# Kernel optimization log

Hardware: AMD Instinct MI355X
Metric: run time of the kernel (lower is better)

The kernel has to match this reference:

```python
import jax, jax.numpy as jnp
import numpy as np

IGNORE_INDEX = 255
THRESH = 0.7
MIN_KEPT = 100000


def _ohem_ce(predict, target):
    # predict: (n, c, h, w) float logits; target: (n, h, w) int labels
    n, c, h, w = predict.shape
    logits = predict.transpose(0, 2, 3, 1).reshape(-1, c)   # (P, c), P = n*h*w
    labels = target.reshape(-1)                              # (P,)

    valid = labels != IGNORE_INDEX
    safe_labels = jnp.where(valid, labels, 0)

    # stable log-softmax once; prob-at-label = exp(logp-at-label)
    logp = jax.nn.log_softmax(logits, axis=-1)               # (P, c)
    logp_lab = jnp.take_along_axis(logp, safe_labels[:, None], axis=-1)[:, 0]  # (P,)
    pred = jnp.exp(logp_lab)                                 # softmax prob of true class

    num_valid = jnp.sum(valid)

    # k-th smallest prob among valid pixels (selection is not differentiated,
    # matching the torch code which does this on numpy/CPU)
    pred_ng = jax.lax.stop_gradient(pred)
    pred_sel = jnp.where(valid, pred_ng, jnp.inf)
    neg_topk, _ = jax.lax.top_k(-pred_sel, MIN_KEPT)         # MIN_KEPT smallest preds
    kth = -neg_topk[-1]                                      # MIN_KEPT-th smallest

    threshold = jnp.where(kth > THRESH, kth, THRESH)

    # OHEM keep rule only applies when num_valid > min_kept; otherwise keep all valid
    do_ohem = num_valid > MIN_KEPT
    kept = jnp.where(do_ohem, valid & (pred_ng <= threshold), valid)

    cnt = jnp.sum(kept)
    # CrossEntropyLoss(mean over non-ignored) on kept pixels
    loss = -jnp.sum(jnp.where(kept, logp_lab, 0.0)) / jnp.maximum(cnt, 1).astype(logp_lab.dtype)
    return loss


def setup_inputs() -> dict:
    key = jax.random.key(0)
    k1, k2 = jax.random.split(key)
    predict = jax.random.normal(k1, (8, 19, 512, 1024), dtype=jnp.float32)
    target = jax.random.randint(k2, (8, 512, 1024), 0, 19, dtype=jnp.int64)
    return {"predict": predict, "target": target}


def reference(predict, target):
    return _ohem_ce(predict, target)
```

## Files before the change

kernel.cpp:

```cpp
#include <hip/hip_runtime.h>
#include <cfloat>
#include <stdint.h>

#define P_TOT     4194304
#define HW_       524288
#define NCLS      19
#define IGNORE_IDX 255
#define MIN_KEPT_ 100000
#define THR       0.7f
#define L2E       1.44269504088896340736f
#define LN2       0.69314718055994530942f

#define SEG_PX    8192
#define NSEG      512

__device__ __forceinline__ double wred_d(double v){
  #pragma unroll
  for (int o = 32; o > 0; o >>= 1) v += __shfl_down(v, o, 64);
  return v;
}
__device__ __forceinline__ unsigned wred_u(unsigned v){
  #pragma unroll
  for (int o = 32; o > 0; o >>= 1) v += __shfl_down(v, o, 64);
  return v;
}

__global__ __launch_bounds__(512) void ohem_pass1(
    const float* __restrict__ logits, const int* __restrict__ tgt,
    double* __restrict__ p_sle, double* __restrict__ p_sva,
    unsigned* __restrict__ p_cnt)
{
  const int t   = threadIdx.x;
  const int seg = blockIdx.x * SEG_PX;
  const int n   = seg >> 19;
  const int r0  = seg & (HW_ - 1);
  const float* plane0 = logits + (size_t)n * (NCLS * (size_t)HW_) + r0;

  int   lab[16];
  float m[16], s[16], g[16];

  #pragma unroll
  for (int j = 0; j < 4; j++){
    int4 tl = *(const int4*)(tgt + seg + j * 2048 + t * 4);
    lab[4*j+0] = tl.x; lab[4*j+1] = tl.y; lab[4*j+2] = tl.z; lab[4*j+3] = tl.w;
  }

  #pragma unroll
  for (int j = 0; j < 4; j++){
    float4 v = *(const float4*)(plane0 + j * 2048 + t * 4);
    float vv[4] = {v.x, v.y, v.z, v.w};
    #pragma unroll
    for (int k = 0; k < 4; k++){
      int p = 4*j + k;
      m[p] = vv[k]; s[p] = 1.0f;
      g[p] = (lab[p] == 0) ? vv[k] : 0.0f;
    }
  }

  #pragma unroll 1
  for (int c = 1; c < NCLS; c += 2){
    const float* pA = plane0 + (size_t)c * HW_;
    const float* pB = pA + HW_;
    float4 va[4], vb[4];
    #pragma unroll
    for (int j = 0; j < 4; j++){
      va[j] = *(const float4*)(pA + j * 2048 + t * 4);
      vb[j] = *(const float4*)(pB + j * 2048 + t * 4);
    }
    #pragma unroll
    for (int j = 0; j < 4; j++){
      float xa[4] = {va[j].x, va[j].y, va[j].z, va[j].w};
      float xb[4] = {vb[j].x, vb[j].y, vb[j].z, vb[j].w};
      #pragma unroll
      for (int k = 0; k < 4; k++){
        int p = 4*j + k;
        float x = xa[k], y = xb[k];
        float mo = m[p];
        float mn = fmaxf(mo, fmaxf(x, y));
        float tt = mn * L2E;
        s[p] = s[p] * __builtin_amdgcn_exp2f(fmaf(mo, L2E, -tt))
             + __builtin_amdgcn_exp2f(fmaf(x, L2E, -tt))
             + __builtin_amdgcn_exp2f(fmaf(y, L2E, -tt));
        m[p] = mn;
        g[p] = (lab[p] == c)     ? x : g[p];
        g[p] = (lab[p] == c + 1) ? y : g[p];
      }
    }
  }

  double sle = 0.0, sva = 0.0; unsigned cnt = 0;
  #pragma unroll
  for (int p = 0; p < 16; p++){
    float lp = (g[p] - m[p]) - __builtin_amdgcn_logf(s[p]) * LN2;
    float pd = __builtin_amdgcn_exp2f(lp * L2E);
    if (lab[p] != IGNORE_IDX){
      cnt += 1u; sva += (double)lp;
      if (pd <= THR){ cnt += 1u << 16; sle += (double)lp; }
    }
  }
  sle = wred_d(sle); sva = wred_d(sva); cnt = wred_u(cnt);

  __shared__ double  ld1[8], ld2[8];
  __shared__ unsigned lc[8];
  int wv = t >> 6, ln = t & 63;
  if (ln == 0){ ld1[wv] = sle; ld2[wv] = sva; lc[wv] = cnt; }
  __syncthreads();
  if (t == 0){
    double a = 0, b = 0; unsigned c2 = 0;
    for (int i = 0; i < 8; i++){ a += ld1[i]; b += ld2[i]; c2 += lc[i]; }
    p_sle[blockIdx.x] = a; p_sva[blockIdx.x] = b; p_cnt[blockIdx.x] = c2;
  }
}

__global__ __launch_bounds__(1024) void ohem_finish(
    const float* __restrict__ logits, const int* __restrict__ tgt,
    const double* __restrict__ p_sle, const double* __restrict__ p_sva,
    const unsigned* __restrict__ p_cnt,
    unsigned* __restrict__ keys, float* __restrict__ logp,
    float* __restrict__ out)
{
  __shared__ double  rs1[16], rs2[16];
  __shared__ unsigned rc1[16], rc2[16];
  __shared__ unsigned s_flag, s_prefix, s_rank;
  __shared__ unsigned s_hist[4096];

  int t = threadIdx.x;
  double sle = 0.0, sva = 0.0; unsigned cle = 0, cva = 0;
  for (int i = t; i < NSEG; i += 1024){
    sle += p_sle[i]; sva += p_sva[i];
    unsigned c = p_cnt[i];
    cva += c & 0xFFFFu; cle += c >> 16;
  }
  sle = wred_d(sle); sva = wred_d(sva);
  cle = wred_u(cle); cva = wred_u(cva);
  int wv = t >> 6, ln = t & 63;
  if (ln == 0){ rs1[wv] = sle; rs2[wv] = sva; rc1[wv] = cle; rc2[wv] = cva; }
  __syncthreads();
  if (t == 0){
    double S1 = 0, S2 = 0; unsigned C1 = 0, C2 = 0;
    for (int i = 0; i < 16; i++){ S1 += rs1[i]; S2 += rs2[i]; C1 += rc1[i]; C2 += rc2[i]; }
    unsigned flag;
    if (C2 <= MIN_KEPT_){
      unsigned d = C2 > 1u ? C2 : 1u;
      out[0] = (float)(-S2 / (double)d);
      flag = 0;
    } else if (C1 >= MIN_KEPT_){
      out[0] = (float)(-S1 / (double)C1);
      flag = 0;
    } else flag = 1;
    s_flag = flag;
  }
  __syncthreads();
  if (!s_flag) return;

  for (int p = t; p < P_TOT; p += 1024){
    int n = p >> 19; int r = p & (HW_ - 1);
    const float* bp = logits + (size_t)n * (NCLS * (size_t)HW_) + r;
    int lab = tgt[p];
    int lv  = (lab != IGNORE_IDX);
    int ls  = lv ? lab : 0;
    float mxv = -FLT_MAX, va[NCLS];
    #pragma unroll
    for (int c = 0; c < NCLS; c++){
      float x = bp[(size_t)c * HW_];
      va[c] = x; mxv = fmaxf(mxv, x);
    }
    float xlv = va[0];
    #pragma unroll
    for (int c = 1; c < NCLS; c++) if (c == ls) xlv = va[c];
    float sev = 0.f;
    #pragma unroll
    for (int c = 0; c < NCLS; c++) sev += __expf(va[c] - mxv);
    float lp = (xlv - mxv) - __logf(sev);
    float pd = __expf(lp);
    keys[p] = lv ? __float_as_uint(pd) : 0xFFFFFFFFu;
    logp[p] = lp;
  }
  __syncthreads();

  unsigned prefix = 0, rank = MIN_KEPT_;
  #pragma unroll
  for (int rd = 0; rd < 3; rd++){
    const int sh = (rd == 0) ? 20 : (rd == 1) ? 8 : 0;
    const int nb = (rd == 2) ? 8 : 12;
    const unsigned nbin = 1u << nb;
    for (unsigned i = t; i < nbin; i += 1024) s_hist[i] = 0;
    __syncthreads();
    for (int p = t; p < P_TOT; p += 1024){
      unsigned k = keys[p];
      unsigned hi = (rd == 0) ? 0u : (k >> (sh + nb));
      if (hi == prefix) atomicAdd(&s_hist[(k >> sh) & (nbin - 1)], 1u);
    }
    __syncthreads();
    if (t == 0){
      unsigned cum = 0, b = 0;
      for (; b < nbin - 1; b++){
        unsigned cc = s_hist[b];
        if (cum + cc >= rank) break;
        cum += cc;
      }
      s_prefix = (prefix << nb) | b;
      s_rank = rank - cum;
    }
    __syncthreads();
    prefix = s_prefix; rank = s_rank;
    __syncthreads();
  }
  unsigned kb = prefix;

  double s = 0.0; unsigned c = 0;
  for (int p = t; p < P_TOT; p += 1024){
    unsigned k = keys[p];
    if (k <= kb){ c++; s += (double)logp[p]; }
  }
  s = wred_d(s); c = wred_u(c);
  if (ln == 0){ rs1[wv] = s; rc1[wv] = c; }
  __syncthreads();
  if (t == 0){
    double S = 0; unsigned CC = 0;
    for (int i = 0; i < 16; i++){ S += rs1[i]; CC += rc1[i]; }
    unsigned d = CC > 1u ? CC : 1u;
    out[0] = (float)(-S / (double)d);
  }
}

extern "C" void kernel_launch(void* const* d_in, const int* in_sizes, int n_in,
                              void* d_out, int out_size, void* d_ws, size_t ws_size,
                              hipStream_t stream)
{
  const float* logits = (const float*)d_in[0];
  const int*   tgt    = (const int*)d_in[1];
  float* out = (float*)d_out;

  double*   p_sle = (double*)d_ws;
  double*   p_sva = p_sle + NSEG;
  unsigned* p_cnt = (unsigned*)(p_sva + NSEG);
  unsigned* keys  = p_cnt + NSEG;
  float*    logp  = (float*)(keys + P_TOT);

  hipLaunchKernelGGL(ohem_pass1, dim3(NSEG), dim3(512), 0, stream,
                     logits, tgt, p_sle, p_sva, p_cnt);
  hipLaunchKernelGGL(ohem_finish, dim3(1), dim3(1024), 0, stream,
                     logits, tgt, p_sle, p_sva, p_cnt, keys, logp, out);
}
```

Baseline: 425.3 us.

## Halve per-block segment and double-buffer class-pair loads in pass1

Each pass1 block now covers 4096 pixels instead of 8192, giving 1024 blocks, and each thread holds 8 pixels instead of 16. Launch bounds ask for 4 blocks per CU. The class loop is fully unrolled with two register buffers, so the loads for the next class pair are issued while the current pair is computed. The goal is more occupancy and memory-level parallelism in this bandwidth-bound streaming pass, at the cost of twice as many partials for the finish kernel to reduce.

```diff
diff --git a/kernel.cpp b/kernel.cpp
--- a/kernel.cpp
+++ b/kernel.cpp
@@ -11,8 +11,8 @@
 #define L2E       1.44269504088896340736f
 #define LN2       0.69314718055994530942f
 
-#define SEG_PX    8192
-#define NSEG      512
+#define SEG_PX    4096
+#define NSEG      1024
 
 __device__ __forceinline__ double wred_d(double v){
   #pragma unroll
@@ -25,7 +25,7 @@
   return v;
 }
 
-__global__ __launch_bounds__(512) void ohem_pass1(
+__global__ __launch_bounds__(512, 4) void ohem_pass1(
     const float* __restrict__ logits, const int* __restrict__ tgt,
     double* __restrict__ p_sle, double* __restrict__ p_sva,
     unsigned* __restrict__ p_cnt)
@@ -36,17 +36,17 @@
   const int r0  = seg & (HW_ - 1);
   const float* plane0 = logits + (size_t)n * (NCLS * (size_t)HW_) + r0;
 
-  int   lab[16];
-  float m[16], s[16], g[16];
-
-  #pragma unroll
-  for (int j = 0; j < 4; j++){
+  int   lab[8];
+  float m[8], s[8], g[8];
+
+  #pragma unroll
+  for (int j = 0; j < 2; j++){
     int4 tl = *(const int4*)(tgt + seg + j * 2048 + t * 4);
     lab[4*j+0] = tl.x; lab[4*j+1] = tl.y; lab[4*j+2] = tl.z; lab[4*j+3] = tl.w;
   }
 
   #pragma unroll
-  for (int j = 0; j < 4; j++){
+  for (int j = 0; j < 2; j++){
     float4 v = *(const float4*)(plane0 + j * 2048 + t * 4);
     float vv[4] = {v.x, v.y, v.z, v.w};
     #pragma unroll
@@ -57,40 +57,56 @@
     }
   }
 
-  #pragma unroll 1
-  for (int c = 1; c < NCLS; c += 2){
-    const float* pA = plane0 + (size_t)c * HW_;
-    const float* pB = pA + HW_;
-    float4 va[4], vb[4];
-    #pragma unroll
-    for (int j = 0; j < 4; j++){
-      va[j] = *(const float4*)(pA + j * 2048 + t * 4);
-      vb[j] = *(const float4*)(pB + j * 2048 + t * 4);
-    }
-    #pragma unroll
-    for (int j = 0; j < 4; j++){
-      float xa[4] = {va[j].x, va[j].y, va[j].z, va[j].w};
-      float xb[4] = {vb[j].x, vb[j].y, vb[j].z, vb[j].w};
-      #pragma unroll
-      for (int k = 0; k < 4; k++){
-        int p = 4*j + k;
-        float x = xa[k], y = xb[k];
-        float mo = m[p];
-        float mn = fmaxf(mo, fmaxf(x, y));
-        float tt = mn * L2E;
-        s[p] = s[p] * __builtin_amdgcn_exp2f(fmaf(mo, L2E, -tt))
-             + __builtin_amdgcn_exp2f(fmaf(x, L2E, -tt))
-             + __builtin_amdgcn_exp2f(fmaf(y, L2E, -tt));
-        m[p] = mn;
-        g[p] = (lab[p] == c)     ? x : g[p];
-        g[p] = (lab[p] == c + 1) ? y : g[p];
-      }
-    }
-  }
+  float4 vaA[2], vbA[2], vaB[2], vbB[2];
+
+#define LOADPAIR(VA, VB, C) do {                                         \
+    const float* _pA = plane0 + (size_t)(C) * HW_;                       \
+    const float* _pB = _pA + HW_;                                        \
+    _Pragma("unroll")                                                    \
+    for (int j = 0; j < 2; j++){                                         \
+      VA[j] = *(const float4*)(_pA + j * 2048 + t * 4);                  \
+      VB[j] = *(const float4*)(_pB + j * 2048 + t * 4);                  \
+    }                                                                    \
+  } while(0)
+
+#define COMPUTE(VA, VB, C) do {                                          \
+    _Pragma("unroll")                                                    \
+    for (int j = 0; j < 2; j++){                                         \
+      float xa[4] = {VA[j].x, VA[j].y, VA[j].z, VA[j].w};                \
+      float xb[4] = {VB[j].x, VB[j].y, VB[j].z, VB[j].w};                \
+      _Pragma("unroll")                                                  \
+      for (int k = 0; k < 4; k++){                                       \
+        int p = 4*j + k;                                                 \
+        float x = xa[k], y = xb[k];                                      \
+        float mo = m[p];                                                 \
+        float mn = fmaxf(mo, fmaxf(x, y));                               \
+        float tt = mn * L2E;                                             \
+        s[p] = s[p] * __builtin_amdgcn_exp2f(fmaf(mo, L2E, -tt))         \
+             + __builtin_amdgcn_exp2f(fmaf(x, L2E, -tt))                 \
+             + __builtin_amdgcn_exp2f(fmaf(y, L2E, -tt));                \
+        m[p] = mn;                                                       \
+        g[p] = (lab[p] == (C))     ? x : g[p];                           \
+        g[p] = (lab[p] == (C) + 1) ? y : g[p];                           \
+      }                                                                  \
+    }                                                                    \
+  } while(0)
+
+  LOADPAIR(vaA, vbA, 1);
+  #pragma unroll
+  for (int c = 1; c <= 13; c += 4){
+    LOADPAIR(vaB, vbB, c + 2);
+    COMPUTE(vaA, vbA, c);
+    LOADPAIR(vaA, vbA, c + 4);
+    COMPUTE(vaB, vbB, c + 2);
+  }
+  COMPUTE(vaA, vbA, 17);
+
+#undef LOADPAIR
+#undef COMPUTE
 
   double sle = 0.0, sva = 0.0; unsigned cnt = 0;
   #pragma unroll
-  for (int p = 0; p < 16; p++){
+  for (int p = 0; p < 8; p++){
     float lp = (g[p] - m[p]) - __builtin_amdgcn_logf(s[p]) * LN2;
     float pd = __builtin_amdgcn_exp2f(lp * L2E);
     if (lab[p] != IGNORE_IDX){
```

New measurement: 503.4 us. +18.3%, slower.
